# Optimization experiments

Measured on AMD Instinct MI355X. Metric: run time of the kernel, lower is better.

The kernel has to match this reference:

```python
import jax, jax.numpy as jnp
import numpy as np

N = 50000      # query points
M = 50000      # support points
H = 32         # max neighbors
K = 15         # kernel points
CIN = 64
COUT = 128
KP_EXTENT = 0.06
RADIUS = 0.05


def setup_inputs() -> dict:
    key = jax.random.key(0)
    k1, k2, k3, k4, k5, k6, k7 = jax.random.split(key, 7)
    # point coordinates in a small cube so neighbors fall within KP_extent of kernel points
    q_pts = jax.random.uniform(k1, (N, 3), dtype=jnp.float32) * 0.1
    s_pts = jax.random.uniform(k2, (M, 3), dtype=jnp.float32) * 0.1
    # indices in [0, M]; index M selects the shadow (padded) support point
    neighb_inds = jax.random.randint(k3, (N, H), 0, M + 1)
    x = jax.random.normal(k4, (M, CIN), dtype=jnp.float32)
    # kaiming-uniform-like init for [K, Cin, Cout] weights
    weights = jax.random.normal(k5, (K, CIN, COUT), dtype=jnp.float32) / np.sqrt(CIN)
    # kernel points uniformly in a sphere of radius RADIUS, center point fixed at origin
    d = jax.random.normal(k6, (K, 3), dtype=jnp.float32)
    d = d / jnp.linalg.norm(d, axis=1, keepdims=True)
    r = jax.random.uniform(k7, (K, 1), dtype=jnp.float32) ** (1.0 / 3.0) * RADIUS
    kernel_points = (d * r).at[0].set(0.0)
    return {"q_pts": q_pts, "s_pts": s_pts, "x": x, "weights": weights,
            "kernel_points": kernel_points, "neighb_inds": neighb_inds}


def reference(q_pts, s_pts, x, weights, kernel_points, neighb_inds):
    # pad support points with a far-away shadow point (matches torch: +1e6)
    s_pad = jnp.concatenate([s_pts, jnp.full((1, s_pts.shape[1]), 1e6, s_pts.dtype)], axis=0)
    # gather neighbor coords and center on queries: [N, H, 3]
    neighbors = s_pad[neighb_inds] - q_pts[:, None, :]
    # squared distances to each kernel point: [N, H, K]
    diff = neighbors[:, :, None, :] - kernel_points[None, None, :, :]
    sq_d = jnp.sum(diff * diff, axis=3)
    # linear influence, transposed to [N, K, H]
    h = jnp.maximum(1.0 - jnp.sqrt(sq_d) / KP_EXTENT, 0.0)
    h = jnp.swapaxes(h, 1, 2)
    # pad features with a zero row for shadow neighbors, then gather: [N, H, Cin]
    x_pad = jnp.concatenate([x, jnp.zeros((1, x.shape[1]), x.dtype)], axis=0)
    neighb_x = x_pad[neighb_inds]
    # project features onto kernel points: [N, K, Cin]
    fpk = jnp.einsum('nkh,nhc->nkc', h, neighb_x)
    # per-kernel-point matmul + sum over kernel points: [N, Cout]
    out = jnp.einsum('nkc,kco->no', fpk, weights)
    return out
```

## Files before the change

### kernel.cpp

```cpp
#include <hip/hip_runtime.h>

#define NQ     50000
#define MS     50000
#define NH     32
#define NK     15
#define CIN    64
#define COUT   128
#define QT     16
#define INV_EXT (1.0f/0.06f)

typedef unsigned int   uint32;
typedef unsigned short u16;
typedef _Float16 f16;
typedef _Float16 f16x8 __attribute__((ext_vector_type(8)));
typedef float    f32x4 __attribute__((ext_vector_type(4)));

#define WB_BYTES  (8*32*64*8*2)
#define XPH_BYTES (MS*CIN*2)

__device__ __forceinline__ uint32 permlo(uint32 A, uint32 B) {
#if __has_builtin(__builtin_amdgcn_perm)
    return __builtin_amdgcn_perm(A, B, 0x01000504u);
#else
    return (A & 0xffffu) | (B << 16);
#endif
}
__device__ __forceinline__ uint32 permhi(uint32 A, uint32 B) {
#if __has_builtin(__builtin_amdgcn_perm)
    return __builtin_amdgcn_perm(A, B, 0x03020706u);
#else
    return (A >> 16) | (B & 0xffff0000u);
#endif
}

__device__ __forceinline__ uint32 swA(uint32 o) {
    return o ^ ((((o >> 11) & 7u) ^ ((o >> 7) & 1u)) << 4);
}

__device__ __forceinline__ u16 f16bits(float f) {
    return __builtin_bit_cast(u16, (f16)f);
}

__global__ __launch_bounds__(256)
void xph_pack(const float* __restrict__ x, u16* __restrict__ xph) {
    const int tid = blockIdx.x * 256 + threadIdx.x;
    const int row = tid >> 4;
    const int lp  = tid & 15;
    const float v0 = x[row*CIN +  0 + lp];
    const float v1 = x[row*CIN + 16 + lp];
    const float v2 = x[row*CIN + 32 + lp];
    const float v3 = x[row*CIN + 48 + lp];
    uint2 d;
    d.x = (uint32)f16bits(v0) | ((uint32)f16bits(v1) << 16);
    d.y = (uint32)f16bits(v2) | ((uint32)f16bits(v3) << 16);
    *(uint2*)&xph[row*CIN + lp*4] = d;
}

__global__ __launch_bounds__(64)
void wb_pack(const float* __restrict__ w, u16* __restrict__ wb) {
    const int nt = blockIdx.x >> 5;
    const int ks = blockIdx.x & 31;
    const int l  = threadIdx.x;
    u16 frag[8];
    #pragma unroll
    for (int e = 0; e < 8; ++e) {
        const int Kp = ks*32 + (l >> 4)*8 + e;
        const int c  = Kp >> 4;
        const int k  = Kp & 15;
        const float val = (k < NK) ? w[(k*CIN + c)*COUT + nt*16 + (l & 15)] : 0.0f;
        frag[e] = f16bits(val);
    }
    *(f16x8*)&wb[((nt*32 + ks)*64 + l)*8] = *(f16x8*)frag;
}

__global__ __launch_bounds__(256, 4)
void kpconv_fused(const float* __restrict__ q_pts,
                  const float* __restrict__ s_pts,
                  const u16*  __restrict__ xph,
                  const u16*  __restrict__ wb,
                  const float* __restrict__ kp,
                  const int*   __restrict__ nind,
                  float* __restrict__ out)
{
    __shared__ u16   fpkAT[QT*1024];
    __shared__ float nb[QT*100];
    __shared__ u16   inds[QT*NH];

    const int t  = threadIdx.x;
    const int q0 = blockIdx.x * QT;

    #pragma unroll
    for (int p = t; p < QT*NH; p += 256) {
        const int q = p >> 5, j = p & 31;
        const int ind = nind[(q0 + q)*NH + j];
        const bool valid = (ind < MS);
        inds[p] = (u16)(valid ? ind : 0);
        float sx, sy, sz;
        if (valid) { sx = s_pts[ind*3+0]; sy = s_pts[ind*3+1]; sz = s_pts[ind*3+2]; }
        else       { sx = 1e6f; sy = 1e6f; sz = 1e6f; }
        nb[q*100 + j*3 + 0] = sx - q_pts[(q0+q)*3+0];
        nb[q*100 + j*3 + 1] = sy - q_pts[(q0+q)*3+1];
        nb[q*100 + j*3 + 2] = sz - q_pts[(q0+q)*3+2];
    }
    __syncthreads();

    {
        const int l  = t & 63, wv = t >> 6;
        const int lc = l & 15, lg = l >> 4;
        const int kc = (lc < NK) ? lc : (NK - 1);
        const float kx = kp[kc*3+0], ky = kp[kc*3+1], kz = kp[kc*3+2];
        #pragma unroll
        for (int qi = 0; qi < 4; ++qi) {
            const int q = wv*4 + qi;
            const uint4 iv = *(const uint4*)&inds[q*NH + lg*8];
            uint32 r[8];
            r[0] = iv.x & 0xffffu; r[1] = iv.x >> 16;
            r[2] = iv.y & 0xffffu; r[3] = iv.y >> 16;
            r[4] = iv.z & 0xffffu; r[5] = iv.z >> 16;
            r[6] = iv.w & 0xffffu; r[7] = iv.w >> 16;
            uint2 v0 = *(const uint2*)(xph + r[0]*CIN + lc*4);
            uint2 v1 = *(const uint2*)(xph + r[1]*CIN + lc*4);
            uint2 v2 = *(const uint2*)(xph + r[2]*CIN + lc*4);
            uint2 v3 = *(const uint2*)(xph + r[3]*CIN + lc*4);
            uint2 v4 = *(const uint2*)(xph + r[4]*CIN + lc*4);
            uint2 v5 = *(const uint2*)(xph + r[5]*CIN + lc*4);
            uint2 v6 = *(const uint2*)(xph + r[6]*CIN + lc*4);
            uint2 v7 = *(const uint2*)(xph + r[7]*CIN + lc*4);
            const float* nbq = &nb[q*100 + lg*24];
            const float4 r0 = *(const float4*)(nbq +  0);
            const float4 r1 = *(const float4*)(nbq +  4);
            const float4 r2 = *(const float4*)(nbq +  8);
            const float4 r3 = *(const float4*)(nbq + 12);
            const float4 r4 = *(const float4*)(nbq + 16);
            const float4 r5 = *(const float4*)(nbq + 20);
            float jx[8], jy[8], jz[8];
            jx[0]=r0.x; jy[0]=r0.y; jz[0]=r0.z;
            jx[1]=r0.w; jy[1]=r1.x; jz[1]=r1.y;
            jx[2]=r1.z; jy[2]=r1.w; jz[2]=r2.x;
            jx[3]=r2.y; jy[3]=r2.z; jz[3]=r2.w;
            jx[4]=r3.x; jy[4]=r3.y; jz[4]=r3.z;
            jx[5]=r3.w; jy[5]=r4.x; jz[5]=r4.y;
            jx[6]=r4.z; jy[6]=r4.w; jz[6]=r5.x;
            jx[7]=r5.y; jy[7]=r5.z; jz[7]=r5.w;
            u16 hb[8];
            #pragma unroll
            for (int e = 0; e < 8; ++e) {
                const float dx = jx[e] - kx;
                const float dy = jy[e] - ky;
                const float dz = jz[e] - kz;
                float hh = 1.0f - sqrtf(dx*dx + dy*dy + dz*dz) * INV_EXT;
                hh = (hh > 0.0f) ? hh : 0.0f;
                hb[e] = f16bits(hh);
            }
            const f16x8 a = *(const f16x8*)hb;
            f32x4 acc0 = {0,0,0,0}, acc1 = {0,0,0,0}, acc2 = {0,0,0,0}, acc3 = {0,0,0,0};
            #pragma unroll
            for (int ct = 0; ct < 4; ++ct) {
                const uint32 A0 = (ct & 2) ? v0.y : v0.x, B0 = (ct & 2) ? v1.y : v1.x;
                const uint32 A1 = (ct & 2) ? v2.y : v2.x, B1 = (ct & 2) ? v3.y : v3.x;
                const uint32 A2 = (ct & 2) ? v4.y : v4.x, B2 = (ct & 2) ? v5.y : v5.x;
                const uint32 A3 = (ct & 2) ? v6.y : v6.x, B3 = (ct & 2) ? v7.y : v7.x;
                uint4 bd;
                if (ct & 1) {
                    bd.x = permhi(A0, B0); bd.y = permhi(A1, B1);
                    bd.z = permhi(A2, B2); bd.w = permhi(A3, B3);
                } else {
                    bd.x = permlo(A0, B0); bd.y = permlo(A1, B1);
                    bd.z = permlo(A2, B2); bd.w = permlo(A3, B3);
                }
                const f16x8 b = __builtin_bit_cast(f16x8, bd);
                if      (ct == 0) acc0 = __builtin_amdgcn_mfma_f32_16x16x32_f16(a, b, acc0, 0,0,0);
                else if (ct == 1) acc1 = __builtin_amdgcn_mfma_f32_16x16x32_f16(a, b, acc1, 0,0,0);
                else if (ct == 2) acc2 = __builtin_amdgcn_mfma_f32_16x16x32_f16(a, b, acc2, 0,0,0);
                else              acc3 = __builtin_amdgcn_mfma_f32_16x16x32_f16(a, b, acc3, 0,0,0);
            }
            #pragma unroll
            for (int ct = 0; ct < 4; ++ct) {
                const f32x4 av = (ct==0)?acc0:(ct==1)?acc1:(ct==2)?acc2:acc3;
                uint2 dv;
                dv.x = (uint32)f16bits(av[0]) | ((uint32)f16bits(av[1]) << 16);
                dv.y = (uint32)f16bits(av[2]) | ((uint32)f16bits(av[3]) << 16);
                const uint32 o = swA((uint32)(q*2048 + (ct*16 + lc)*32 + lg*8));
                *(uint2*)((char*)fpkAT + o) = dv;
            }
        }
    }
    __syncthreads();

    {
        const int l   = t & 63;
        const int w   = t >> 6;
        const int col = l & 15;
        const int kg  = l >> 4;
        const int nt0 = w * 2;
        f32x4 acc0 = {0.f,0.f,0.f,0.f};
        f32x4 acc1 = {0.f,0.f,0.f,0.f};
        const u16* b0p = wb + (nt0*32)*512 + l*8;
        const u16* b1p = b0p + 32*512;
        const uint32 abase = (uint32)(col*2048 + kg*16);
        #pragma unroll 8
        for (int ks = 0; ks < 32; ++ks) {
            const uint32 aoff = swA(abase + (uint32)(ks*64));
            const f16x8 a  = *(const f16x8*)((const char*)fpkAT + aoff);
            const f16x8 b0 = *(const f16x8*)(b0p + ks*512);
            const f16x8 b1 = *(const f16x8*)(b1p + ks*512);
            acc0 = __builtin_amdgcn_mfma_f32_16x16x32_f16(a, b0, acc0, 0, 0, 0);
            acc1 = __builtin_amdgcn_mfma_f32_16x16x32_f16(a, b1, acc1, 0, 0, 0);
        }
        const int rbase = kg * 4;
        #pragma unroll
        for (int r = 0; r < 4; ++r) {
            out[(q0 + rbase + r)*COUT + nt0*16 + col]      = acc0[r];
            out[(q0 + rbase + r)*COUT + nt0*16 + 16 + col] = acc1[r];
        }
    }
}

extern "C" void kernel_launch(void* const* d_in, const int* in_sizes, int n_in,
                              void* d_out, int out_size, void* d_ws, size_t ws_size,
                              hipStream_t stream) {
    const float* q_pts = (const float*)d_in[0];
    const float* s_pts = (const float*)d_in[1];
    const float* x     = (const float*)d_in[2];
    const float* wts   = (const float*)d_in[3];
    const float* kp    = (const float*)d_in[4];
    const int*   nind  = (const int*)d_in[5];
    float* out = (float*)d_out;

    u16* wbp = (u16*)d_ws;
    u16* xph = (u16*)((char*)d_ws + WB_BYTES);

    hipLaunchKernelGGL(xph_pack, dim3(3125), dim3(256), 0, stream, x, xph);
    hipLaunchKernelGGL(wb_pack,  dim3(256),  dim3(64),  0, stream, wts, wbp);
    hipLaunchKernelGGL(kpconv_fused, dim3(NQ/QT), dim3(256), 0, stream,
                       q_pts, s_pts, xph, wbp, kp, nind, out);
}
```

Measured before the change: 74.18 us.

## Merge pack kernels, hoist feature gathers, and use packed f16 conversion

Merges the x and weight packing kernels into one launch to save a kernel launch and its tail. In the fused kernel, all 32 neighbor feature gathers for the four queries are issued up front so their global-load latency overlaps with the influence computation. Float-to-half conversions now use the packed round-toward-zero instruction, and the square root uses the hardware builtin. The costs are higher register pressure from holding the gathered features and slightly different rounding (RTZ, and a less precise sqrt).

Measured after the change: 67.24 us. -9.4%, faster.

```diff
diff --git a/kernel.cpp b/kernel.cpp
--- a/kernel.cpp
+++ b/kernel.cpp
@@ -18,6 +18,12 @@
 #define WB_BYTES  (8*32*64*8*2)
 #define XPH_BYTES (MS*CIN*2)
 
+#if __has_builtin(__builtin_amdgcn_sqrtf)
+#define SQRTF __builtin_amdgcn_sqrtf
+#else
+#define SQRTF sqrtf
+#endif
+
 __device__ __forceinline__ uint32 permlo(uint32 A, uint32 B) {
 #if __has_builtin(__builtin_amdgcn_perm)
     return __builtin_amdgcn_perm(A, B, 0x01000504u);
@@ -33,44 +39,54 @@
 #endif
 }
 
+__device__ __forceinline__ u16 f16bits(float f) {
+    return __builtin_bit_cast(u16, (f16)f);
+}
+
+__device__ __forceinline__ uint32 pk2(float a, float b) {
+#if __has_builtin(__builtin_amdgcn_cvt_pkrtz)
+    return __builtin_bit_cast(uint32, __builtin_amdgcn_cvt_pkrtz(a, b));
+#else
+    return (uint32)f16bits(a) | ((uint32)f16bits(b) << 16);
+#endif
+}
+
 __device__ __forceinline__ uint32 swA(uint32 o) {
     return o ^ ((((o >> 11) & 7u) ^ ((o >> 7) & 1u)) << 4);
 }
 
-__device__ __forceinline__ u16 f16bits(float f) {
-    return __builtin_bit_cast(u16, (f16)f);
-}
-
 __global__ __launch_bounds__(256)
-void xph_pack(const float* __restrict__ x, u16* __restrict__ xph) {
-    const int tid = blockIdx.x * 256 + threadIdx.x;
-    const int row = tid >> 4;
-    const int lp  = tid & 15;
-    const float v0 = x[row*CIN +  0 + lp];
-    const float v1 = x[row*CIN + 16 + lp];
-    const float v2 = x[row*CIN + 32 + lp];
-    const float v3 = x[row*CIN + 48 + lp];
-    uint2 d;
-    d.x = (uint32)f16bits(v0) | ((uint32)f16bits(v1) << 16);
-    d.y = (uint32)f16bits(v2) | ((uint32)f16bits(v3) << 16);
-    *(uint2*)&xph[row*CIN + lp*4] = d;
-}
-
-__global__ __launch_bounds__(64)
-void wb_pack(const float* __restrict__ w, u16* __restrict__ wb) {
-    const int nt = blockIdx.x >> 5;
-    const int ks = blockIdx.x & 31;
-    const int l  = threadIdx.x;
-    u16 frag[8];
-    #pragma unroll
-    for (int e = 0; e < 8; ++e) {
-        const int Kp = ks*32 + (l >> 4)*8 + e;
-        const int c  = Kp >> 4;
-        const int k  = Kp & 15;
-        const float val = (k < NK) ? w[(k*CIN + c)*COUT + nt*16 + (l & 15)] : 0.0f;
-        frag[e] = f16bits(val);
-    }
-    *(f16x8*)&wb[((nt*32 + ks)*64 + l)*8] = *(f16x8*)frag;
+void pack_all(const float* __restrict__ x, u16* __restrict__ xph,
+              const float* __restrict__ w, u16* __restrict__ wb) {
+    const int bid = blockIdx.x;
+    if (bid < 3125) {
+        const int tid = bid * 256 + threadIdx.x;
+        const int row = tid >> 4;
+        const int lp  = tid & 15;
+        const float v0 = x[row*CIN +  0 + lp];
+        const float v1 = x[row*CIN + 16 + lp];
+        const float v2 = x[row*CIN + 32 + lp];
+        const float v3 = x[row*CIN + 48 + lp];
+        uint2 d;
+        d.x = pk2(v0, v1);
+        d.y = pk2(v2, v3);
+        *(uint2*)&xph[row*CIN + lp*4] = d;
+    } else {
+        const int u  = (bid - 3125) * 4 + (threadIdx.x >> 6);
+        const int nt = u >> 5;
+        const int ks = u & 31;
+        const int l  = threadIdx.x & 63;
+        u16 frag[8];
+        #pragma unroll
+        for (int e = 0; e < 8; ++e) {
+            const int Kp = ks*32 + (l >> 4)*8 + e;
+            const int c  = Kp >> 4;
+            const int k  = Kp & 15;
+            const float val = (k < NK) ? w[(k*CIN + c)*COUT + nt*16 + (l & 15)] : 0.0f;
+            frag[e] = f16bits(val);
+        }
+        *(f16x8*)&wb[((nt*32 + ks)*64 + l)*8] = *(f16x8*)frag;
+    }
 }
 
 __global__ __launch_bounds__(256, 4)
@@ -109,6 +125,8 @@
         const int lc = l & 15, lg = l >> 4;
         const int kc = (lc < NK) ? lc : (NK - 1);
         const float kx = kp[kc*3+0], ky = kp[kc*3+1], kz = kp[kc*3+2];
+
+        uint2 v[4][8];
         #pragma unroll
         for (int qi = 0; qi < 4; ++qi) {
             const int q = wv*4 + qi;
@@ -118,14 +136,14 @@
             r[2] = iv.y & 0xffffu; r[3] = iv.y >> 16;
             r[4] = iv.z & 0xffffu; r[5] = iv.z >> 16;
             r[6] = iv.w & 0xffffu; r[7] = iv.w >> 16;
-            uint2 v0 = *(const uint2*)(xph + r[0]*CIN + lc*4);
-            uint2 v1 = *(const uint2*)(xph + r[1]*CIN + lc*4);
-            uint2 v2 = *(const uint2*)(xph + r[2]*CIN + lc*4);
-            uint2 v3 = *(const uint2*)(xph + r[3]*CIN + lc*4);
-            uint2 v4 = *(const uint2*)(xph + r[4]*CIN + lc*4);
-            uint2 v5 = *(const uint2*)(xph + r[5]*CIN + lc*4);
-            uint2 v6 = *(const uint2*)(xph + r[6]*CIN + lc*4);
-            uint2 v7 = *(const uint2*)(xph + r[7]*CIN + lc*4);
+            #pragma unroll
+            for (int e = 0; e < 8; ++e)
+                v[qi][e] = *(const uint2*)(xph + r[e]*CIN + lc*4);
+        }
+
+        #pragma unroll
+        for (int qi = 0; qi < 4; ++qi) {
+            const int q = wv*4 + qi;
             const float* nbq = &nb[q*100 + lg*24];
             const float4 r0 = *(const float4*)(nbq +  0);
             const float4 r1 = *(const float4*)(nbq +  4);
@@ -142,24 +160,26 @@
             jx[5]=r3.w; jy[5]=r4.x; jz[5]=r4.y;
             jx[6]=r4.z; jy[6]=r4.w; jz[6]=r5.x;
             jx[7]=r5.y; jy[7]=r5.z; jz[7]=r5.w;
-            u16 hb[8];
+            float hh[8];
             #pragma unroll
             for (int e = 0; e < 8; ++e) {
                 const float dx = jx[e] - kx;
                 const float dy = jy[e] - ky;
                 const float dz = jz[e] - kz;
-                float hh = 1.0f - sqrtf(dx*dx + dy*dy + dz*dz) * INV_EXT;
-                hh = (hh > 0.0f) ? hh : 0.0f;
-                hb[e] = f16bits(hh);
+                float h = 1.0f - SQRTF(dx*dx + dy*dy + dz*dz) * INV_EXT;
+                hh[e] = (h > 0.0f) ? h : 0.0f;
             }
-            const f16x8 a = *(const f16x8*)hb;
+            uint32 ab[4];
+            ab[0] = pk2(hh[0], hh[1]); ab[1] = pk2(hh[2], hh[3]);
+            ab[2] = pk2(hh[4], hh[5]); ab[3] = pk2(hh[6], hh[7]);
+            const f16x8 a = __builtin_bit_cast(f16x8, *(uint4*)ab);
             f32x4 acc0 = {0,0,0,0}, acc1 = {0,0,0,0}, acc2 = {0,0,0,0}, acc3 = {0,0,0,0};
             #pragma unroll
             for (int ct = 0; ct < 4; ++ct) {
-                const uint32 A0 = (ct & 2) ? v0.y : v0.x, B0 = (ct & 2) ? v1.y : v1.x;
-                const uint32 A1 = (ct & 2) ? v2.y : v2.x, B1 = (ct & 2) ? v3.y : v3.x;
-                const uint32 A2 = (ct & 2) ? v4.y : v4.x, B2 = (ct & 2) ? v5.y : v5.x;
-                const uint32 A3 = (ct & 2) ? v6.y : v6.x, B3 = (ct & 2) ? v7.y : v7.x;
+                const uint32 A0 = (ct & 2) ? v[qi][0].y : v[qi][0].x, B0 = (ct & 2) ? v[qi][1].y : v[qi][1].x;
+                const uint32 A1 = (ct & 2) ? v[qi][2].y : v[qi][2].x, B1 = (ct & 2) ? v[qi][3].y : v[qi][3].x;
+                const uint32 A2 = (ct & 2) ? v[qi][4].y : v[qi][4].x, B2 = (ct & 2) ? v[qi][5].y : v[qi][5].x;
+                const uint32 A3 = (ct & 2) ? v[qi][6].y : v[qi][6].x, B3 = (ct & 2) ? v[qi][7].y : v[qi][7].x;
                 uint4 bd;
                 if (ct & 1) {
                     bd.x = permhi(A0, B0); bd.y = permhi(A1, B1);
@@ -178,8 +198,8 @@
             for (int ct = 0; ct < 4; ++ct) {
                 const f32x4 av = (ct==0)?acc0:(ct==1)?acc1:(ct==2)?acc2:acc3;
                 uint2 dv;
-                dv.x = (uint32)f16bits(av[0]) | ((uint32)f16bits(av[1]) << 16);
-                dv.y = (uint32)f16bits(av[2]) | ((uint32)f16bits(av[3]) << 16);
+                dv.x = pk2(av[0], av[1]);
+                dv.y = pk2(av[2], av[3]);
                 const uint32 o = swA((uint32)(q*2048 + (ct*16 + lc)*32 + lg*8));
                 *(uint2*)((char*)fpkAT + o) = dv;
             }
@@ -230,8 +250,7 @@
     u16* wbp = (u16*)d_ws;
     u16* xph = (u16*)((char*)d_ws + WB_BYTES);
 
-    hipLaunchKernelGGL(xph_pack, dim3(3125), dim3(256), 0, stream, x, xph);
-    hipLaunchKernelGGL(wb_pack,  dim3(256),  dim3(64),  0, stream, wts, wbp);
+    hipLaunchKernelGGL(pack_all, dim3(3125 + 64), dim3(256), 0, stream, x, xph, wts, wbp);
     hipLaunchKernelGGL(kpconv_fused, dim3(NQ/QT), dim3(256), 0, stream,
                        q_pts, s_pts, xph, wbp, kp, nind, out);
 }
```
